# Performance work log

Measured on AMD Instinct MI355X. Metric: run time of the kernel, lower is better.

The kernel has to match this reference:

```python
import jax, jax.numpy as jnp
import numpy as np
from jax import lax

B, A, H, W = 64, 8, 64, 128
T_EXP = 32
ACTION_HORIZON = 64
DS = 1.0          # reward_cfg['ds']
TEMPERATURE = 0.1 # policy_kwargs['temperature'], method='sharpen'
FOV_HALF_ANGLE_DEG = 35.0
FOV_MAX_RANGE = 100


def _build_buffers():
    # per-action 3x3 one-hot transition kernels: weight 1.0 at 'center' cell,
    # 0.0 at left/right cells (as in MaxEntIRL.__init__ with policy_method='pp')
    center = [[2, 2], [2, 1], [2, 0], [1, 2], [1, 0], [0, 2], [0, 1], [0, 0]]
    tp = np.zeros((A, 1, 3, 3), np.float32)
    for i, (r, c) in enumerate(center):
        tp[i, 0, r, c] = 1.0
    # trapezoidal FOV mask built on a (2H, W) grid, then cropped to first H rows
    rows = np.arange(2 * H, dtype=np.float32)[:, None]
    cols = np.arange(W, dtype=np.float32)[None, :]
    half = np.tan(np.deg2rad(FOV_HALF_ANGLE_DEG)) * rows
    mask = ((np.abs(cols - (W - 1) / 2.0) <= half) & (rows <= FOV_MAX_RANGE))
    fov = mask.astype(np.float32)[:H][None, None]  # (1,1,H,W)
    dyn = np.array([[-1, -1], [-1, 0], [-1, 1], [0, -1],
                    [0, 1], [1, -1], [1, 0], [1, 1]], np.int32)
    return jnp.asarray(tp), jnp.asarray(fov), jnp.asarray(dyn)


def setup_inputs() -> dict:
    key = jax.random.key(0)
    k1, k2 = jax.random.split(key)
    policy = jax.random.normal(k1, (B, A, H, W), jnp.float32)
    # expert SE(2)-like poses; only [:, :, :2, 2] translations are read.
    # Scale to [0,100) so grid cells spread over the map before clamping.
    expert = jax.random.uniform(k2, (B, T_EXP, 3, 3), jnp.float32) * 100.0
    tp, fov, dyn = _build_buffers()
    return {"policy": policy, "expert": expert, "transition_probs": tp,
            "fov_mask": fov, "dynamics": dyn, "action_horizon": ACTION_HORIZON}


def reference(policy, expert, transition_probs, fov_mask, dynamics, action_horizon):
    Bn, An, Hn, Wn = policy.shape
    n_states = Hn * Wn
    barange = jnp.arange(Bn)

    # expert poses -> clamped grid cells  (S: (B, T, 2))
    S = jnp.floor_divide(expert[:, :, :2, 2], DS).astype(jnp.int32)
    S = jnp.stack([jnp.clip(S[..., 0], 0, Hn - 1),
                   jnp.clip(S[..., 1], 0, Wn - 1)], axis=-1)

    # earliest pose inside FOV (argmax of bool gives first True, else 0)
    mask2d = fov_mask[0, 0]
    in_fov = mask2d[S[..., 0], S[..., 1]] > 0  # (B, T)
    idx0 = jnp.argmax(in_fov, axis=1)
    S0c = S[barange, idx0]     # (B, 2) start cell
    S1c = S[:, -1]             # (B, 2) terminal cell
    S0 = S0c[:, 0] * Wn + S0c[:, 1]
    S1 = S1c[:, 0] * Wn + S1c[:, 1]

    # sharpen policy over action dim (stable softmax with temperature)
    logits = (policy - jnp.max(policy, axis=1, keepdims=True)) / TEMPERATURE
    policy_2d = jax.nn.softmax(logits, axis=1)  # (B, A, H, W)

    mu0 = jnp.zeros((Bn, n_states), jnp.float32).at[barange, S0].set(1.0)

    def step(carry, _):
        prev, total = carry
        # zero_terminal_state: kill visitation mass at the terminal cell
        prev_z = prev.at[barange, S1].set(0.0)
        pm = policy_2d * prev_z.reshape(Bn, 1, Hn, Wn)  # (B, A, H, W)
        new = lax.conv_general_dilated(
            pm, transition_probs, window_strides=(1, 1),
            padding=[(1, 1), (1, 1)],
            dimension_numbers=("NCHW", "OIHW", "NCHW"),
            feature_group_count=An)
        new = jnp.sum(new, axis=1).reshape(Bn, n_states)
        return (new, total + prev_z), None

    (last, total), _ = lax.scan(step, (mu0, jnp.zeros_like(mu0)),
                                None, length=action_horizon - 1)
    mu = (total + last).reshape(Bn, Hn, Wn)

    # greedy rollout (torch runs this under no_grad)
    policy_flat = policy.reshape(Bn, An, n_states)
    most_likely_action = jnp.argmax(policy_flat, axis=1)  # (B, n_states)
    most_likely_action = lax.stop_gradient(most_likely_action)

    def roll(St, _):
        a = most_likely_action[barange, St]
        coord = jnp.stack([St // Wn, St % Wn], axis=1) + dynamics[a]
        coord = jnp.stack([jnp.clip(coord[:, 0], 0, Hn - 1),
                           jnp.clip(coord[:, 1], 0, Wn - 1)], axis=1)
        return coord[:, 0] * Wn + coord[:, 1], coord

    _, coords = lax.scan(roll, S0, None, length=action_horizon - 1)  # (T-1,B,2)
    states = jnp.concatenate([S0c[None].astype(coords.dtype), coords],
                             axis=0).transpose(1, 0, 2)  # (B, T, 2)
    bidx = jnp.broadcast_to(barange[:, None], (Bn, action_horizon))
    states_grid = jnp.zeros((Bn, Hn, Wn), jnp.float32).at[
        bidx, states[..., 0], states[..., 1]].add(1.0)
    return mu, states_grid, states
```

## Files before the change

kernel.cpp:

```cpp
#include <hip/hip_runtime.h>

#define THREADS 512

typedef unsigned int u32;
typedef unsigned long long u64;

constexpr int BN = 64, AN = 8, HN = 64, WN = 128;
constexpr int HWN = HN * WN;
constexpr int TEXP = 32, AH = 64;
constexpr size_t LDS_BYTES = (size_t)AN * HWN * 2;

constexpr int GYc[8] = { 1, 1, 1, 0, 0, -1, -1, -1 };
constexpr int GXc[8] = { 1, 0, -1, 1, -1, 1, 0, -1 };

typedef _Float16 h2 __attribute__((ext_vector_type(2)));
union U { u32 u; h2 p; _Float16 h[2]; };

__device__ __forceinline__ h2  H(u32 x) { U t; t.u = x; return t.p; }
__device__ __forceinline__ u32 Bc(h2 x) { U t; t.p = x; return t.u; }

__device__ __forceinline__ u32 ab16(u32 hi, u32 lo) {
    return (u32)((((u64)hi << 32) | lo) >> 16);
}
__device__ __forceinline__ u32 wsr1(u32 x) {
    return (u32)__builtin_amdgcn_update_dpp(0, (int)x, 0x138, 0xf, 0xf, true);
}
__device__ __forceinline__ u32 wsl1(u32 x) {
    return (u32)__builtin_amdgcn_update_dpp(0, (int)x, 0x130, 0xf, 0xf, true);
}
__device__ __forceinline__ u32 shL(u32 d) { return ab16(d, wsr1(d)); }
__device__ __forceinline__ u32 shR(u32 d) { return ab16(wsl1(d), d); }

extern "C" __global__ __launch_bounds__(THREADS, 2)
void maxent_fused(const float* __restrict__ policy,
                  const float* __restrict__ expert,
                  const float* __restrict__ fovm,
                  const int*   __restrict__ dyn,
                  float* __restrict__ out)
{
    (void)dyn;
    extern __shared__ char smem[];
    const int tid  = threadIdx.x;
    const int lane = tid & 63;
    const bool isScan = blockIdx.x < BN;
    const int b = isScan ? (int)blockIdx.x : (int)blockIdx.x - BN;

    int Sr = 0, Sc = 0; bool infov = false;
    if (lane < TEXP) {
        float e0 = expert[b * (TEXP * 9) + lane * 9 + 2];
        float e1 = expert[b * (TEXP * 9) + lane * 9 + 5];
        int r = (int)floorf(e0); r = r < 0 ? 0 : (r > HN - 1 ? HN - 1 : r);
        int c = (int)floorf(e1); c = c < 0 ? 0 : (c > WN - 1 ? WN - 1 : c);
        Sr = r; Sc = c;
        infov = fovm[r * WN + c] > 0.0f;
    }
    unsigned long long fmask = __ballot(infov);
    int idx0 = fmask ? (__ffsll(fmask) - 1) : 0;
    const int S0r = __shfl(Sr, idx0), S0c = __shfl(Sc, idx0);
    const int S1r = __shfl(Sr, TEXP - 1), S1c = __shfl(Sc, TEXP - 1);
    const bool S0eqS1 = (S0r == S1r) && (S0c == S1c);

    if (isScan) {
        _Float16* Pl = (_Float16*)smem;

        const float* pb = policy + (size_t)b * AN * HWN;
        #pragma unroll
        for (int kk = 0; kk < 4; ++kk) {
            const int pix = (kk * THREADS + tid) * 4;
            float v[8][4];
            float m[4] = {-3.4e38f, -3.4e38f, -3.4e38f, -3.4e38f};
            #pragma unroll
            for (int a = 0; a < 8; ++a) {
                float4 f = *(const float4*)(pb + a * HWN + pix);
                v[a][0] = f.x; v[a][1] = f.y; v[a][2] = f.z; v[a][3] = f.w;
                m[0] = fmaxf(m[0], f.x); m[1] = fmaxf(m[1], f.y);
                m[2] = fmaxf(m[2], f.z); m[3] = fmaxf(m[3], f.w);
            }
            float s[4] = {0.f, 0.f, 0.f, 0.f};
            #pragma unroll
            for (int a = 0; a < 8; ++a)
                #pragma unroll
                for (int j = 0; j < 4; ++j) { v[a][j] = __expf((v[a][j] - m[j]) * 10.0f); s[j] += v[a][j]; }
            float inv[4];
            #pragma unroll
            for (int j = 0; j < 4; ++j) inv[j] = 1.0f / s[j];
            #pragma unroll
            for (int a = 0; a < 8; ++a) {
                u32 lo = (u32)__builtin_bit_cast(unsigned short, (_Float16)(v[a][0] * inv[0]))
                       | ((u32)__builtin_bit_cast(unsigned short, (_Float16)(v[a][1] * inv[1])) << 16);
                u32 hi = (u32)__builtin_bit_cast(unsigned short, (_Float16)(v[a][2] * inv[2]))
                       | ((u32)__builtin_bit_cast(unsigned short, (_Float16)(v[a][3] * inv[3])) << 16);
                uint2 pk2; pk2.x = lo; pk2.y = hi;
                *(uint2*)(Pl + a * HWN + pix) = pk2;
            }
        }
        __syncthreads();

        const int w = tid >> 6;
        const int rbase = 8 * w;

        u32 pa[8][8];
        #pragma unroll
        for (int a = 0; a < 8; ++a) {
            const int gy = GYc[a], gx = GXc[a];
            #pragma unroll
            for (int r = 0; r < 8; ++r) {
                const int sr = rbase + r + gy;
                u32 d = 0;
                if (sr >= 0 && sr < HN)
                    d = *(const u32*)(Pl + a * HWN + sr * WN + 2 * lane);
                pa[a][r] = (gx == 0) ? d : ((gx == 1) ? shR(d) : shL(d));
            }
        }
        __syncthreads();

        u32* hx = (u32*)smem;
        for (int i = tid; i < 2048; i += THREADS) hx[i] = 0;

        u32 s[8], zm[8];
        #pragma unroll
        for (int r = 0; r < 8; ++r) {
            const int gr = rbase + r;
            s[r] = (!S0eqS1 && gr == S0r && (S0c >> 1) == lane)
                     ? ((S0c & 1) ? 0x3C000000u : 0x00003C00u) : 0u;
            zm[r] = ~0u;
            if (gr == S1r && (S1c >> 1) == lane)
                zm[r] = (S1c & 1) ? 0x0000FFFFu : 0xFFFF0000u;
        }
        __syncthreads();
        hx[(2 * w + 0) * 64 + lane] = s[0];
        hx[(2 * w + 1) * 64 + lane] = s[7];
        __syncthreads();

        u32 t16[8], nn[8];
        float tot[16];
        #pragma unroll
        for (int r = 0; r < 8; ++r) { t16[r] = 0; nn[r] = 0; }
        #pragma unroll
        for (int k = 0; k < 16; ++k) tot[k] = 0.f;

        const int rdT = (2 * w - 1) * 64 + lane;
        const int rdD = (2 * w + 2) * 64 + lane;
        const int wr0 = (2 * w + 0) * 64 + lane;
        const int wr7 = (2 * w + 1) * 64 + lane;

        for (int it = 0; it < AH - 1; ++it) {
            const int pb_ = (it & 1) << 10;
            const int wb_ = 1024 - pb_;
            const bool active = (rbase <= S0r + it + 1) && (rbase + 7 >= S0r - it - 1);
            if (active) {
                const u32 hT = (w > 0) ? hx[pb_ + rdT] : 0u;
                const u32 hD = (w < 7) ? hx[pb_ + rdD] : 0u;

                #pragma unroll
                for (int r = 0; r < 8; ++r) t16[r] = Bc(H(t16[r]) + H(s[r]));
                if ((it & 3) == 3 || it == AH - 2) {
                    #pragma unroll
                    for (int r = 0; r < 8; ++r) {
                        tot[2*r]   += (float)H(t16[r]).x;
                        tot[2*r+1] += (float)H(t16[r]).y;
                        t16[r] = 0;
                    }
                }

                u32 L[8], R[8];
                #pragma unroll
                for (int r = 0; r < 8; ++r) { L[r] = shL(s[r]); R[r] = shR(s[r]); }

                u32 ns[8];
                constexpr int RO[8] = {1, 2, 3, 4, 5, 6, 0, 7};
                #pragma unroll
                for (int ri = 0; ri < 8; ++ri) {
                    const int r = RO[ri];
                    const u32 cm1 = (r == 0) ? hT      : s[r - 1];
                    const u32 lm1 = (r == 0) ? shL(hT) : L[r - 1];
                    const u32 rm1 = (r == 0) ? shR(hT) : R[r - 1];
                    const u32 cp1 = (r == 7) ? hD      : s[r + 1];
                    const u32 lp1 = (r == 7) ? shL(hD) : L[r + 1];
                    const u32 rp1 = (r == 7) ? shR(hD) : R[r + 1];
                    h2 acc =  H(pa[0][r]) * H(rp1);
                    acc += H(pa[1][r]) * H(cp1);
                    acc += H(pa[2][r]) * H(lp1);
                    acc += H(pa[3][r]) * H(R[r]);
                    acc += H(pa[4][r]) * H(L[r]);
                    acc += H(pa[5][r]) * H(rm1);
                    acc += H(pa[6][r]) * H(cm1);
                    acc += H(pa[7][r]) * H(lm1);
                    nn[r] = Bc(acc);
                    ns[r] = nn[r] & zm[r];
                }
                #pragma unroll
                for (int r = 0; r < 8; ++r) s[r] = ns[r];

                hx[wb_ + wr0] = s[0];
                hx[wb_ + wr7] = s[7];
            }
            __syncthreads();
        }

        #pragma unroll
        for (int r = 0; r < 8; ++r) {
            float2 f;
            f.x = tot[2*r]   + (float)H(nn[r]).x;
            f.y = tot[2*r+1] + (float)H(nn[r]).y;
            *(float2*)(out + (size_t)b * HWN + (rbase + r) * WN + 2 * lane) = f;
        }

    } else {
        short* amap = (short*)smem;
        float* grid = (float*)(smem + 16384);
        const float* pb = policy + (size_t)b * AN * HWN;
        #pragma unroll
        for (int c = 0; c < 4; ++c) {
            const int pix = (c * THREADS + tid) * 4;
            float4 f0 = *(const float4*)(pb + pix);
            float b0 = f0.x, b1 = f0.y, b2 = f0.z, b3 = f0.w;
            int a0 = 0, a1 = 0, a2 = 0, a3 = 0;
            #pragma unroll
            for (int a = 1; a < 8; ++a) {
                float4 f = *(const float4*)(pb + a * HWN + pix);
                if (f.x > b0) { b0 = f.x; a0 = a; }
                if (f.y > b1) { b1 = f.y; a1 = a; }
                if (f.z > b2) { b2 = f.z; a2 = a; }
                if (f.w > b3) { b3 = f.w; a3 = a; }
            }
            uint2 pk2;
            pk2.x = (u32)a0 | ((u32)a1 << 16);
            pk2.y = (u32)a2 | ((u32)a3 << 16);
            *(uint2*)(amap + pix) = pk2;
        }
        for (int i = tid; i < HWN; i += THREADS) grid[i] = 0.f;
        __syncthreads();

        if (tid == 0) {
            float* so = out + 2 * (size_t)HWN * BN + b * (AH * 2);
            int cr = S0r, cc = S0c;
            so[0] = (float)cr; so[1] = (float)cc;
            grid[cr * WN + cc] += 1.0f;
            for (int t = 1; t < AH; ++t) {
                const int a = amap[cr * WN + cc];
                const int dr = (a < 3) ? -1 : ((a < 5) ? 0 : 1);
                int dc;
                if (a < 3) dc = a - 1;
                else if (a == 3) dc = -1;
                else if (a == 4) dc = 1;
                else dc = a - 6;
                cr += dr; cc += dc;
                cr = cr < 0 ? 0 : (cr > HN - 1 ? HN - 1 : cr);
                cc = cc < 0 ? 0 : (cc > WN - 1 ? WN - 1 : cc);
                so[t * 2] = (float)cr; so[t * 2 + 1] = (float)cc;
                grid[cr * WN + cc] += 1.0f;
            }
        }
        __syncthreads();
        float* sg = out + (size_t)HWN * BN + b * HWN;
        for (int i = tid; i < HWN; i += THREADS) sg[i] = grid[i];
    }
}

extern "C" void kernel_launch(void* const* d_in, const int* in_sizes, int n_in,
                              void* d_out, int out_size, void* d_ws, size_t ws_size,
                              hipStream_t stream) {
    const float* policy = (const float*)d_in[0];
    const float* expert = (const float*)d_in[1];
    const float* fovm   = (const float*)d_in[3];
    const int*   dyn    = (const int*)d_in[4];
    float* out = (float*)d_out;

    (void)hipFuncSetAttribute((const void*)maxent_fused,
                              hipFuncAttributeMaxDynamicSharedMemorySize,
                              (int)LDS_BYTES);
    hipLaunchKernelGGL(maxent_fused, dim3(2 * BN), dim3(THREADS), LDS_BYTES, stream,
                       policy, expert, fovm, dyn, out);
}
```

Before: 49.01 us.

## Use 3-row ghost halos to run three stencil steps per barrier

Each wave now exchanges three halo rows with its neighbours instead of one and performs three propagation substeps per exchange, with redundant computation on the overlapping ghost rows. This cuts block-wide __syncthreads and LDS halo round-trips by about a factor of three across the 63-step loop. In exchange it holds more policy rows in registers (12 per action) and does extra FMA work on ghost rows, which increases register pressure.

```diff
diff --git a/kernel.cpp b/kernel.cpp
--- a/kernel.cpp
+++ b/kernel.cpp
@@ -8,6 +8,7 @@
 constexpr int BN = 64, AN = 8, HN = 64, WN = 128;
 constexpr int HWN = HN * WN;
 constexpr int TEXP = 32, AH = 64;
+constexpr int NPER = 21;
 constexpr size_t LDS_BYTES = (size_t)AN * HWN * 2;
 
 constexpr int GYc[8] = { 1, 1, 1, 0, 0, -1, -1, -1 };
@@ -99,37 +100,42 @@
         const int w = tid >> 6;
         const int rbase = 8 * w;
 
-        u32 pa[8][8];
+        u32 pa[8][12];
         #pragma unroll
         for (int a = 0; a < 8; ++a) {
             const int gy = GYc[a], gx = GXc[a];
             #pragma unroll
-            for (int r = 0; r < 8; ++r) {
-                const int sr = rbase + r + gy;
+            for (int j = 0; j < 12; ++j) {
+                const int sr = rbase + j - 2 + gy;
                 u32 d = 0;
                 if (sr >= 0 && sr < HN)
                     d = *(const u32*)(Pl + a * HWN + sr * WN + 2 * lane);
-                pa[a][r] = (gx == 0) ? d : ((gx == 1) ? shR(d) : shL(d));
+                pa[a][j] = (gx == 0) ? d : ((gx == 1) ? shR(d) : shL(d));
             }
         }
         __syncthreads();
 
         u32* hx = (u32*)smem;
-        for (int i = tid; i < 2048; i += THREADS) hx[i] = 0;
-
-        u32 s[8], zm[8];
-        #pragma unroll
-        for (int r = 0; r < 8; ++r) {
-            const int gr = rbase + r;
-            s[r] = (!S0eqS1 && gr == S0r && (S0c >> 1) == lane)
-                     ? ((S0c & 1) ? 0x3C000000u : 0x00003C00u) : 0u;
-            zm[r] = ~0u;
+        for (int i = tid; i < 6144; i += THREADS) hx[i] = 0;
+
+        u32 x[14], zm[14];
+        #pragma unroll
+        for (int i = 0; i < 14; ++i) {
+            const int gr = rbase + i - 3;
+            x[i] = 0;
+            if (i >= 3 && i <= 10)
+                x[i] = (!S0eqS1 && gr == S0r && (S0c >> 1) == lane)
+                         ? ((S0c & 1) ? 0x3C000000u : 0x00003C00u) : 0u;
+            zm[i] = ~0u;
             if (gr == S1r && (S1c >> 1) == lane)
-                zm[r] = (S1c & 1) ? 0x0000FFFFu : 0xFFFF0000u;
-        }
-        __syncthreads();
-        hx[(2 * w + 0) * 64 + lane] = s[0];
-        hx[(2 * w + 1) * 64 + lane] = s[7];
+                zm[i] = (S1c & 1) ? 0x0000FFFFu : 0xFFFF0000u;
+        }
+        __syncthreads();
+        #pragma unroll
+        for (int i = 0; i < 3; ++i) {
+            hx[w * 384 + i * 64 + lane]       = x[3 + i];
+            hx[w * 384 + (3 + i) * 64 + lane] = x[8 + i];
+        }
         __syncthreads();
 
         u32 t16[8], nn[8];
@@ -139,64 +145,62 @@
         #pragma unroll
         for (int k = 0; k < 16; ++k) tot[k] = 0.f;
 
-        const int rdT = (2 * w - 1) * 64 + lane;
-        const int rdD = (2 * w + 2) * 64 + lane;
-        const int wr0 = (2 * w + 0) * 64 + lane;
-        const int wr7 = (2 * w + 1) * 64 + lane;
-
-        for (int it = 0; it < AH - 1; ++it) {
-            const int pb_ = (it & 1) << 10;
-            const int wb_ = 1024 - pb_;
-            const bool active = (rbase <= S0r + it + 1) && (rbase + 7 >= S0r - it - 1);
+        #define SUBSTEP(LO, HI, SAVE)                                            \
+        {                                                                        \
+            _Pragma("unroll")                                                    \
+            for (int r = 0; r < 8; ++r) t16[r] = Bc(H(t16[r]) + H(x[r + 3]));    \
+            u32 Lx[14], Rx[14], y[14];                                           \
+            _Pragma("unroll")                                                    \
+            for (int i = (LO) + 2; i <= (HI) + 4; ++i) {                         \
+                Lx[i] = shL(x[i]); Rx[i] = shR(x[i]);                            \
+            }                                                                    \
+            _Pragma("unroll")                                                    \
+            for (int r = (LO); r <= (HI); ++r) {                                 \
+                h2 acc =  H(pa[0][r + 2]) * H(Rx[r + 4]);                        \
+                acc += H(pa[1][r + 2]) * H(x [r + 4]);                           \
+                acc += H(pa[2][r + 2]) * H(Lx[r + 4]);                           \
+                acc += H(pa[3][r + 2]) * H(Rx[r + 3]);                           \
+                acc += H(pa[4][r + 2]) * H(Lx[r + 3]);                           \
+                acc += H(pa[5][r + 2]) * H(Rx[r + 2]);                           \
+                acc += H(pa[6][r + 2]) * H(x [r + 2]);                           \
+                acc += H(pa[7][r + 2]) * H(Lx[r + 2]);                           \
+                u32 un = Bc(acc);                                                \
+                if ((SAVE) && r >= 0 && r <= 7) nn[r] = un;                      \
+                y[r + 3] = un & zm[r + 3];                                       \
+            }                                                                    \
+            _Pragma("unroll")                                                    \
+            for (int r = (LO); r <= (HI); ++r) x[r + 3] = y[r + 3];              \
+        }
+
+        for (int pp = 0; pp < NPER; ++pp) {
+            const int rd = (pp & 1) ? 3072 : 0;
+            const int wr = 3072 - rd;
+            const int rad = 3 * pp + 4;
+            const bool active = (rbase <= S0r + rad) && (rbase + 7 >= S0r - rad);
             if (active) {
-                const u32 hT = (w > 0) ? hx[pb_ + rdT] : 0u;
-                const u32 hD = (w < 7) ? hx[pb_ + rdD] : 0u;
-
-                #pragma unroll
-                for (int r = 0; r < 8; ++r) t16[r] = Bc(H(t16[r]) + H(s[r]));
-                if ((it & 3) == 3 || it == AH - 2) {
-                    #pragma unroll
-                    for (int r = 0; r < 8; ++r) {
-                        tot[2*r]   += (float)H(t16[r]).x;
-                        tot[2*r+1] += (float)H(t16[r]).y;
-                        t16[r] = 0;
-                    }
+                #pragma unroll
+                for (int i = 0; i < 3; ++i) {
+                    x[i]      = (w > 0) ? hx[rd + (w - 1) * 384 + (3 + i) * 64 + lane] : 0u;
+                    x[11 + i] = (w < 7) ? hx[rd + (w + 1) * 384 + i * 64 + lane] : 0u;
                 }
-
-                u32 L[8], R[8];
-                #pragma unroll
-                for (int r = 0; r < 8; ++r) { L[r] = shL(s[r]); R[r] = shR(s[r]); }
-
-                u32 ns[8];
-                constexpr int RO[8] = {1, 2, 3, 4, 5, 6, 0, 7};
-                #pragma unroll
-                for (int ri = 0; ri < 8; ++ri) {
-                    const int r = RO[ri];
-                    const u32 cm1 = (r == 0) ? hT      : s[r - 1];
-                    const u32 lm1 = (r == 0) ? shL(hT) : L[r - 1];
-                    const u32 rm1 = (r == 0) ? shR(hT) : R[r - 1];
-                    const u32 cp1 = (r == 7) ? hD      : s[r + 1];
-                    const u32 lp1 = (r == 7) ? shL(hD) : L[r + 1];
-                    const u32 rp1 = (r == 7) ? shR(hD) : R[r + 1];
-                    h2 acc =  H(pa[0][r]) * H(rp1);
-                    acc += H(pa[1][r]) * H(cp1);
-                    acc += H(pa[2][r]) * H(lp1);
-                    acc += H(pa[3][r]) * H(R[r]);
-                    acc += H(pa[4][r]) * H(L[r]);
-                    acc += H(pa[5][r]) * H(rm1);
-                    acc += H(pa[6][r]) * H(cm1);
-                    acc += H(pa[7][r]) * H(lm1);
-                    nn[r] = Bc(acc);
-                    ns[r] = nn[r] & zm[r];
+                SUBSTEP(-2, 9, false);
+                SUBSTEP(-1, 8, false);
+                SUBSTEP(0, 7, true);
+                #pragma unroll
+                for (int r = 0; r < 8; ++r) {
+                    tot[2*r]   += (float)H(t16[r]).x;
+                    tot[2*r+1] += (float)H(t16[r]).y;
+                    t16[r] = 0;
                 }
                 #pragma unroll
-                for (int r = 0; r < 8; ++r) s[r] = ns[r];
-
-                hx[wb_ + wr0] = s[0];
-                hx[wb_ + wr7] = s[7];
+                for (int i = 0; i < 3; ++i) {
+                    hx[wr + w * 384 + i * 64 + lane]       = x[3 + i];
+                    hx[wr + w * 384 + (3 + i) * 64 + lane] = x[8 + i];
+                }
             }
             __syncthreads();
         }
+        #undef SUBSTEP
 
         #pragma unroll
         for (int r = 0; r < 8; ++r) {
```

New measurement: 50.69 us. +3.4%, slower.

## Double block size to 1024 threads, four rows per wave in stencil scan

Applied to the files above, without the earlier changes.

Raises the block to 1024 threads, so each of 16 waves owns 4 grid rows instead of 8. This halves the serial per-iteration stencil work per wave in the 63-step scan and the per-thread register footprint. The halo buffer grows to match, and the 8-term FMA chain is split into two accumulators for more ILP. In exchange, each of the 63 barriers now synchronizes 16 waves, and the launch-bounds occupancy hint is dropped.

```diff
diff --git a/kernel.cpp b/kernel.cpp
--- a/kernel.cpp
+++ b/kernel.cpp
@@ -1,6 +1,6 @@
 #include <hip/hip_runtime.h>
 
-#define THREADS 512
+#define THREADS 1024
 
 typedef unsigned int u32;
 typedef unsigned long long u64;
@@ -31,7 +31,7 @@
 __device__ __forceinline__ u32 shL(u32 d) { return ab16(d, wsr1(d)); }
 __device__ __forceinline__ u32 shR(u32 d) { return ab16(wsl1(d), d); }
 
-extern "C" __global__ __launch_bounds__(THREADS, 2)
+extern "C" __global__ __launch_bounds__(THREADS)
 void maxent_fused(const float* __restrict__ policy,
                   const float* __restrict__ expert,
                   const float* __restrict__ fovm,
@@ -65,7 +65,7 @@
 
         const float* pb = policy + (size_t)b * AN * HWN;
         #pragma unroll
-        for (int kk = 0; kk < 4; ++kk) {
+        for (int kk = 0; kk < 2; ++kk) {
             const int pix = (kk * THREADS + tid) * 4;
             float v[8][4];
             float m[4] = {-3.4e38f, -3.4e38f, -3.4e38f, -3.4e38f};
@@ -97,14 +97,14 @@
         __syncthreads();
 
         const int w = tid >> 6;
-        const int rbase = 8 * w;
-
-        u32 pa[8][8];
+        const int rbase = 4 * w;
+
+        u32 pa[8][4];
         #pragma unroll
         for (int a = 0; a < 8; ++a) {
             const int gy = GYc[a], gx = GXc[a];
             #pragma unroll
-            for (int r = 0; r < 8; ++r) {
+            for (int r = 0; r < 4; ++r) {
                 const int sr = rbase + r + gy;
                 u32 d = 0;
                 if (sr >= 0 && sr < HN)
@@ -115,91 +115,93 @@
         __syncthreads();
 
         u32* hx = (u32*)smem;
-        for (int i = tid; i < 2048; i += THREADS) hx[i] = 0;
-
-        u32 s[8], zm[8];
-        #pragma unroll
-        for (int r = 0; r < 8; ++r) {
+        for (int i = tid; i < 4096; i += THREADS) hx[i] = 0;
+
+        u32 x[6], zm[4];
+        #pragma unroll
+        for (int r = 0; r < 4; ++r) {
             const int gr = rbase + r;
-            s[r] = (!S0eqS1 && gr == S0r && (S0c >> 1) == lane)
-                     ? ((S0c & 1) ? 0x3C000000u : 0x00003C00u) : 0u;
+            x[1 + r] = (!S0eqS1 && gr == S0r && (S0c >> 1) == lane)
+                         ? ((S0c & 1) ? 0x3C000000u : 0x00003C00u) : 0u;
             zm[r] = ~0u;
             if (gr == S1r && (S1c >> 1) == lane)
                 zm[r] = (S1c & 1) ? 0x0000FFFFu : 0xFFFF0000u;
         }
-        __syncthreads();
-        hx[(2 * w + 0) * 64 + lane] = s[0];
-        hx[(2 * w + 1) * 64 + lane] = s[7];
-        __syncthreads();
-
-        u32 t16[8], nn[8];
-        float tot[16];
-        #pragma unroll
-        for (int r = 0; r < 8; ++r) { t16[r] = 0; nn[r] = 0; }
-        #pragma unroll
-        for (int k = 0; k < 16; ++k) tot[k] = 0.f;
+        x[0] = 0; x[5] = 0;
+        __syncthreads();
+        hx[(2 * w + 0) * 64 + lane] = x[1];
+        hx[(2 * w + 1) * 64 + lane] = x[4];
+        __syncthreads();
+
+        u32 t16[4], nn[4];
+        float tot[8];
+        #pragma unroll
+        for (int r = 0; r < 4; ++r) { t16[r] = 0; nn[r] = 0; }
+        #pragma unroll
+        for (int k = 0; k < 8; ++k) tot[k] = 0.f;
 
         const int rdT = (2 * w - 1) * 64 + lane;
         const int rdD = (2 * w + 2) * 64 + lane;
         const int wr0 = (2 * w + 0) * 64 + lane;
-        const int wr7 = (2 * w + 1) * 64 + lane;
+        const int wr3 = (2 * w + 1) * 64 + lane;
 
         for (int it = 0; it < AH - 1; ++it) {
-            const int pb_ = (it & 1) << 10;
-            const int wb_ = 1024 - pb_;
-            const bool active = (rbase <= S0r + it + 1) && (rbase + 7 >= S0r - it - 1);
+            const int pb_ = (it & 1) << 11;
+            const int wb_ = 2048 - pb_;
+            const bool active = (rbase <= S0r + it + 1) && (rbase + 3 >= S0r - it - 1);
             if (active) {
-                const u32 hT = (w > 0) ? hx[pb_ + rdT] : 0u;
-                const u32 hD = (w < 7) ? hx[pb_ + rdD] : 0u;
-
-                #pragma unroll
-                for (int r = 0; r < 8; ++r) t16[r] = Bc(H(t16[r]) + H(s[r]));
+                const u32 hT = (w > 0)  ? hx[pb_ + rdT] : 0u;
+                const u32 hD = (w < 15) ? hx[pb_ + rdD] : 0u;
+
+                #pragma unroll
+                for (int r = 0; r < 4; ++r) t16[r] = Bc(H(t16[r]) + H(x[1 + r]));
                 if ((it & 3) == 3 || it == AH - 2) {
                     #pragma unroll
-                    for (int r = 0; r < 8; ++r) {
+                    for (int r = 0; r < 4; ++r) {
                         tot[2*r]   += (float)H(t16[r]).x;
                         tot[2*r+1] += (float)H(t16[r]).y;
                         t16[r] = 0;
                     }
                 }
 
-                u32 L[8], R[8];
-                #pragma unroll
-                for (int r = 0; r < 8; ++r) { L[r] = shL(s[r]); R[r] = shR(s[r]); }
-
-                u32 ns[8];
-                constexpr int RO[8] = {1, 2, 3, 4, 5, 6, 0, 7};
-                #pragma unroll
-                for (int ri = 0; ri < 8; ++ri) {
+                u32 L[6], R[6];
+                #pragma unroll
+                for (int i = 1; i <= 4; ++i) { L[i] = shL(x[i]); R[i] = shR(x[i]); }
+
+                u32 ns[4];
+                constexpr int RO[4] = {1, 2, 0, 3};
+                #pragma unroll
+                for (int ri = 0; ri < 4; ++ri) {
                     const int r = RO[ri];
-                    const u32 cm1 = (r == 0) ? hT      : s[r - 1];
-                    const u32 lm1 = (r == 0) ? shL(hT) : L[r - 1];
-                    const u32 rm1 = (r == 0) ? shR(hT) : R[r - 1];
-                    const u32 cp1 = (r == 7) ? hD      : s[r + 1];
-                    const u32 lp1 = (r == 7) ? shL(hD) : L[r + 1];
-                    const u32 rp1 = (r == 7) ? shR(hD) : R[r + 1];
-                    h2 acc =  H(pa[0][r]) * H(rp1);
-                    acc += H(pa[1][r]) * H(cp1);
-                    acc += H(pa[2][r]) * H(lp1);
-                    acc += H(pa[3][r]) * H(R[r]);
-                    acc += H(pa[4][r]) * H(L[r]);
-                    acc += H(pa[5][r]) * H(rm1);
-                    acc += H(pa[6][r]) * H(cm1);
-                    acc += H(pa[7][r]) * H(lm1);
-                    nn[r] = Bc(acc);
-                    ns[r] = nn[r] & zm[r];
+                    const u32 cm1 = (r == 0) ? hT      : x[r];
+                    const u32 lm1 = (r == 0) ? shL(hT) : L[r];
+                    const u32 rm1 = (r == 0) ? shR(hT) : R[r];
+                    const u32 cp1 = (r == 3) ? hD      : x[r + 2];
+                    const u32 lp1 = (r == 3) ? shL(hD) : L[r + 2];
+                    const u32 rp1 = (r == 3) ? shR(hD) : R[r + 2];
+                    h2 acc0 =  H(pa[0][r]) * H(rp1);
+                    acc0 += H(pa[1][r]) * H(cp1);
+                    acc0 += H(pa[2][r]) * H(lp1);
+                    acc0 += H(pa[3][r]) * H(R[r + 1]);
+                    h2 acc1 =  H(pa[4][r]) * H(L[r + 1]);
+                    acc1 += H(pa[5][r]) * H(rm1);
+                    acc1 += H(pa[6][r]) * H(cm1);
+                    acc1 += H(pa[7][r]) * H(lm1);
+                    const u32 un = Bc(acc0 + acc1);
+                    nn[r] = un;
+                    ns[r] = un & zm[r];
                 }
                 #pragma unroll
-                for (int r = 0; r < 8; ++r) s[r] = ns[r];
-
-                hx[wb_ + wr0] = s[0];
-                hx[wb_ + wr7] = s[7];
+                for (int r = 0; r < 4; ++r) x[1 + r] = ns[r];
+
+                hx[wb_ + wr0] = x[1];
+                hx[wb_ + wr3] = x[4];
             }
             __syncthreads();
         }
 
         #pragma unroll
-        for (int r = 0; r < 8; ++r) {
+        for (int r = 0; r < 4; ++r) {
             float2 f;
             f.x = tot[2*r]   + (float)H(nn[r]).x;
             f.y = tot[2*r+1] + (float)H(nn[r]).y;
@@ -211,7 +213,7 @@
         float* grid = (float*)(smem + 16384);
         const float* pb = policy + (size_t)b * AN * HWN;
         #pragma unroll
-        for (int c = 0; c < 4; ++c) {
+        for (int c = 0; c < 2; ++c) {
             const int pix = (c * THREADS + tid) * 4;
             float4 f0 = *(const float4*)(pb + pix);
             float b0 = f0.x, b1 = f0.y, b2 = f0.z, b3 = f0.w;
```

After: 49.32 us. No clear change (+0.6%).
